# Optimization experiments

Measured on AMD Instinct MI355X. Metric: run time of the kernel, lower is better.

The kernel has to match this reference:

```python
import jax, jax.numpy as jnp
import numpy as np

B, L, D, H, A, NLAYERS, P = 16, 512, 768, 4, 100, 2, 3
DK = A // H  # 25
EPS = 1e-6


def setup_inputs() -> dict:
    key = jax.random.key(0)
    ks = jax.random.split(key, 20)
    s = 0.02
    return {
        "sequence_output": jax.random.normal(ks[0], (B, L, D), jnp.float32),
        "syntax_matrix": jax.random.normal(ks[1], (B, H, L, L), jnp.float32),
        # LayerNorm params
        "ln_a": jnp.ones((D,), jnp.float32),
        "ln_b": jnp.zeros((D,), jnp.float32),
        # Wxx: bert_dim -> attdim
        "Wxx_w": jax.random.normal(ks[2], (A, D), jnp.float32) * s,
        "Wxx_b": jnp.zeros((A,), jnp.float32),
        # attention q/k projections (attdim -> attdim)
        "q_w": jax.random.normal(ks[3], (A, A), jnp.float32) * s,
        "q_b": jnp.zeros((A,), jnp.float32),
        "k_w": jax.random.normal(ks[4], (A, A), jnp.float32) * s,
        "k_b": jnp.zeros((A,), jnp.float32),
        # W: attdim -> attdim
        "W_w": jax.random.normal(ks[5], (A, A), jnp.float32) * s,
        "W_b": jnp.zeros((A,), jnp.float32),
        # Wx: (H + 2*attdim) -> H
        "Wx_w": jax.random.normal(ks[6], (H, H + 2 * A), jnp.float32) * s,
        "Wx_b": jnp.zeros((H,), jnp.float32),
        # aggregate_W: attdim*(layers+1) -> attdim
        "agg_w": jax.random.normal(ks[7], (A, A * (NLAYERS + 1)), jnp.float32) * s,
        "agg_b": jnp.zeros((A,), jnp.float32),
        # classifier: 100 -> polarities_dim
        "cls_w": jax.random.normal(ks[8], (P, A), jnp.float32) * s,
        "cls_b": jnp.zeros((P,), jnp.float32),
        # masks (ints)
        "mask_ids": jnp.ones((B, L), jnp.int32),
        "src_mask": jnp.ones((B, L), jnp.int32),
    }


def reference(sequence_output, syntax_matrix, ln_a, ln_b, Wxx_w, Wxx_b,
              q_w, q_b, k_w, k_b, W_w, W_b, Wx_w, Wx_b,
              agg_w, agg_b, cls_w, cls_b, mask_ids, src_mask):
    # custom LayerNorm: torch.std is unbiased (ddof=1)
    mean = sequence_output.mean(-1, keepdims=True)
    std = jnp.std(sequence_output, axis=-1, ddof=1, keepdims=True)
    seq = ln_a * (sequence_output - mean) / (std + EPS) + ln_b

    # Wxx projection to attdim (dropout = identity in eval)
    x = seq @ Wxx_w.T + Wxx_b  # [B, L, A]

    # multi-head attention producing adjacency [B, H, L, L]
    q = (x @ q_w.T + q_b).reshape(B, L, H, DK).transpose(0, 2, 1, 3)
    k = (x @ k_w.T + k_b).reshape(B, L, H, DK).transpose(0, 2, 1, 3)
    scores = jnp.einsum('bhid,bhjd->bhij', q, k) / jnp.sqrt(jnp.float32(DK))
    key_mask = src_mask[:, None, None, :]  # [B,1,1,L]
    scores = jnp.where(key_mask == 0, jnp.float32(-1e9), scores)
    scores = scores + syntax_matrix
    adj = jax.nn.softmax(scores, axis=-1)  # [B, H, L, L]

    # split Wx into its adjacency / node-j / node-i blocks so the [B,L,L,H+2A]
    # concat tensor is never materialized (edge MLP is linear => decomposable)
    Aw = Wx_w[:, :H]            # [H, H]
    B1 = Wx_w[:, H:H + A]       # [H, A] applied to x[b, j]
    B2 = Wx_w[:, H + A:]        # [H, A] applied to x[b, i]

    x_g = x
    layer_list = [x]
    for i in range(NLAYERS):
        # Ax = mean over heads of adj_h @ x  (x identical per head)
        Ax = jnp.einsum('bhij,bjd->bid', adj, x_g) / H
        x_g = jax.nn.relu(Ax @ W_w.T + W_b)  # [B, L, A]
        layer_list.append(x_g)
        # edge update: edge[b,g,i,j] = sum_h Aw[g,h]*adj[b,h,i,j]
        e_adj = jnp.einsum('bhij,gh->bgij', adj, Aw)  # [B, H, L, L]
        u = jnp.einsum('bjd,gd->bgj', x_g, B1)        # node1 (index j)
        v = jnp.einsum('bid,gd->bgi', x_g, B2)        # node2 (index i)
        adj = e_adj + u[:, :, None, :] + v[:, :, :, None] + Wx_b[None, :, None, None]

    feats = jnp.concatenate(layer_list, axis=-1)          # [B, L, A*(NLAYERS+1)]
    node = jax.nn.relu(feats @ agg_w.T + agg_b)           # [B, L, A]

    valid_len = jnp.clip(mask_ids.sum(axis=1), 1, None).astype(node.dtype)[:, None]
    pooled = node.sum(axis=1) / valid_len                 # [B, A]
    logits = pooled @ cls_w.T + cls_b                     # [B, P]
    return logits
```

## Files before the change

kernel.cpp:

```cpp
#include <hip/hip_runtime.h>

#define B_ 16
#define L_ 512
#define D_ 768
#define H_ 4
#define A_ 100
#define DK_ 25
#define P_ 3
#define XP_ 128

__global__ __launch_bounds__(256) void k_wprep(const float* __restrict__ Wxx_w,
                                               float* __restrict__ wT)
{
    const int idx = blockIdx.x * 256 + threadIdx.x;
    const int d = idx >> 7, a = idx & 127;
    wT[idx] = (a < A_) ? Wxx_w[(size_t)a * D_ + d] : 0.f;
}

__global__ __launch_bounds__(256) void k_aggprep(const float* __restrict__ agg_w,
                                                 float* __restrict__ aggT)
{
    const int idx = blockIdx.x * 256 + threadIdx.x;
    const int n = idx & 127, k = (idx >> 7) % A_, c = idx / (128 * A_);
    aggT[idx] = (n < A_) ? agg_w[(size_t)n * (3 * A_) + c * A_ + k] : 0.f;
}

__global__ __launch_bounds__(256) void k_qkprep(const float* __restrict__ q_w,
                                                const float* __restrict__ k_w,
                                                float* __restrict__ qkT)
{
    const int idx = blockIdx.x * 256 + threadIdx.x;
    const int n = idx & 255, k = idx >> 8;
    const int half = n >> 7, a = n & 127;
    const float* w = half ? k_w : q_w;
    qkT[idx] = (a < A_) ? w[(size_t)a * A_ + k] : 0.f;
}

__global__ __launch_bounds__(256) void k_wprep2(const float* __restrict__ W_w,
                                                float* __restrict__ WT)
{
    const int idx = blockIdx.x * 256 + threadIdx.x;
    const int n = idx & 127, k = idx >> 7;
    WT[idx] = (n < A_) ? W_w[(size_t)n * A_ + k] : 0.f;
}

__global__ __launch_bounds__(256) void k_lnx(
    const float* __restrict__ seq, const float* __restrict__ ln_a, const float* __restrict__ ln_b,
    const float* __restrict__ wT, const float* __restrict__ Wxx_b, float* __restrict__ xp)
{
    __shared__ float ss[32][36];
    __shared__ float ws[32][128];
    __shared__ float mean_s[32], rd_s[32];
    const int tid = threadIdx.x;
    const int row0 = blockIdx.x * 32;
    const int wv = tid >> 6, lane = tid & 63;

    for (int rr = 0; rr < 8; ++rr) {
        const int r = wv * 8 + rr;
        const float4* src = (const float4*)(seq + (size_t)(row0 + r) * D_);
        float4 a = src[lane], b = src[lane + 64], c = src[lane + 128];
        float s = a.x + a.y + a.z + a.w + b.x + b.y + b.z + b.w + c.x + c.y + c.z + c.w;
        #pragma unroll
        for (int o = 32; o; o >>= 1) s += __shfl_xor(s, o);
        const float m = s * (1.0f / 768.0f);
        float q = (a.x-m)*(a.x-m) + (a.y-m)*(a.y-m) + (a.z-m)*(a.z-m) + (a.w-m)*(a.w-m)
                + (b.x-m)*(b.x-m) + (b.y-m)*(b.y-m) + (b.z-m)*(b.z-m) + (b.w-m)*(b.w-m)
                + (c.x-m)*(c.x-m) + (c.y-m)*(c.y-m) + (c.z-m)*(c.z-m) + (c.w-m)*(c.w-m);
        #pragma unroll
        for (int o = 32; o; o >>= 1) q += __shfl_xor(q, o);
        if (lane == 0) {
            mean_s[r] = m;
            rd_s[r] = 1.0f / (sqrtf(q * (1.0f / 767.0f)) + 1e-6f);
        }
    }
    __syncthreads();

    const int c4 = tid & 31, rg = tid >> 5;
    float4 acc[4];
    #pragma unroll
    for (int i = 0; i < 4; ++i) { acc[i].x = acc[i].y = acc[i].z = acc[i].w = 0.f; }

    for (int kc = 0; kc < 24; ++kc) {
        {
            const int r = tid >> 3, k4 = tid & 7;
            float4 v = *(const float4*)(seq + (size_t)(row0 + r) * D_ + kc * 32 + k4 * 4);
            float4 la = ((const float4*)ln_a)[kc * 8 + k4];
            float4 lb = ((const float4*)ln_b)[kc * 8 + k4];
            const float m = mean_s[r], rd = rd_s[r];
            float4 o;
            o.x = la.x * ((v.x - m) * rd) + lb.x;
            o.y = la.y * ((v.y - m) * rd) + lb.y;
            o.z = la.z * ((v.z - m) * rd) + lb.z;
            o.w = la.w * ((v.w - m) * rd) + lb.w;
            *(float4*)&ss[r][k4 * 4] = o;
        }
        #pragma unroll
        for (int t = 0; t < 4; ++t) {
            const int idx = tid + t * 256;
            const int k = idx >> 5, cc = idx & 31;
            *(float4*)&ws[k][cc * 4] = *(const float4*)(wT + (size_t)(kc * 32 + k) * 128 + cc * 4);
        }
        __syncthreads();
        #pragma unroll 2
        for (int k = 0; k < 32; k += 4) {
            float4 sv[4];
            #pragma unroll
            for (int i = 0; i < 4; ++i) sv[i] = *(float4*)&ss[rg * 4 + i][k];
            #pragma unroll
            for (int j = 0; j < 4; ++j) {
                float4 w4 = *(float4*)&ws[k + j][c4 * 4];
                #pragma unroll
                for (int i = 0; i < 4; ++i) {
                    const float sj = ((float*)&sv[i])[j];
                    acc[i].x += sj * w4.x; acc[i].y += sj * w4.y;
                    acc[i].z += sj * w4.z; acc[i].w += sj * w4.w;
                }
            }
        }
        __syncthreads();
    }

    float4 bias = {0.f, 0.f, 0.f, 0.f};
    if (c4 < 25) bias = ((const float4*)Wxx_b)[c4];
    #pragma unroll
    for (int i = 0; i < 4; ++i) {
        float4 o;
        o.x = acc[i].x + bias.x; o.y = acc[i].y + bias.y;
        o.z = acc[i].z + bias.z; o.w = acc[i].w + bias.w;
        *(float4*)(xp + (size_t)(row0 + rg * 4 + i) * XP_ + c4 * 4) = o;
    }
}

__global__ __launch_bounds__(256) void k_qkg(
    const float* __restrict__ xp, const float* __restrict__ qkT,
    const float* __restrict__ q_b, const float* __restrict__ k_b,
    float* __restrict__ qt, float* __restrict__ kt)
{
    __shared__ float ss[32][104];
    __shared__ float ws[A_][128];
    const int tid = threadIdx.x;
    const int row0 = blockIdx.x * 32;
    const int half = blockIdx.y;
    const int c4 = tid & 31, rg = tid >> 5;

    for (int idx = tid; idx < 32 * 25; idx += 256) {
        const int r = idx / 25, k4 = idx % 25;
        *(float4*)&ss[r][k4 * 4] = *(const float4*)(xp + (size_t)(row0 + r) * XP_ + k4 * 4);
    }
    for (int idx = tid; idx < A_ * 32; idx += 256) {
        const int k = idx >> 5, cc = idx & 31;
        *(float4*)&ws[k][cc * 4] = *(const float4*)(qkT + (size_t)k * 256 + half * 128 + cc * 4);
    }
    __syncthreads();

    float4 acc[4];
    #pragma unroll
    for (int i = 0; i < 4; ++i) { acc[i].x = acc[i].y = acc[i].z = acc[i].w = 0.f; }
    #pragma unroll 5
    for (int k = 0; k < A_; k += 4) {
        float4 sv[4];
        #pragma unroll
        for (int i = 0; i < 4; ++i) sv[i] = *(float4*)&ss[rg * 4 + i][k];
        #pragma unroll
        for (int j = 0; j < 4; ++j) {
            float4 w4 = *(float4*)&ws[k + j][c4 * 4];
            #pragma unroll
            for (int i = 0; i < 4; ++i) {
                const float sj = ((float*)&sv[i])[j];
                acc[i].x += sj * w4.x; acc[i].y += sj * w4.y;
                acc[i].z += sj * w4.z; acc[i].w += sj * w4.w;
            }
        }
    }

    if (c4 < 25) {
        const float4 bias = ((const float4*)(half ? k_b : q_b))[c4];
        float* dst = half ? kt : qt;
        #pragma unroll
        for (int i = 0; i < 4; ++i) {
            float4 o;
            o.x = acc[i].x + bias.x; o.y = acc[i].y + bias.y;
            o.z = acc[i].z + bias.z; o.w = acc[i].w + bias.w;
            *(float4*)(dst + (size_t)(row0 + rg * 4 + i) * A_ + c4 * 4) = o;
        }
    }
}

__global__ __launch_bounds__(256) void k_sgemm(
    const float* __restrict__ qt, const float* __restrict__ kt,
    const float* __restrict__ syn, const int* __restrict__ src_mask,
    float* __restrict__ es)
{
    __shared__ float qs[DK_][64];
    __shared__ float ks[DK_][64];
    __shared__ int ms[64];
    const int tid = threadIdx.x;
    const int bh = blockIdx.z;
    const int b = bh >> 2, h = bh & 3;
    const int i0 = blockIdx.x * 64, j0 = blockIdx.y * 64;
    const float* qbase = qt + ((size_t)b * L_ + i0) * A_ + h * DK_;
    const float* kbase = kt + ((size_t)b * L_ + j0) * A_ + h * DK_;
    {
        const int r = tid >> 2, c = tid & 3;
        #pragma unroll
        for (int k = 0; k < 7; ++k) {
            const int d = c + 4 * k;
            if (d < DK_) {
                qs[d][r] = qbase[(size_t)r * A_ + d];
                ks[d][r] = kbase[(size_t)r * A_ + d];
            }
        }
        if (tid < 64) ms[tid] = src_mask[b * L_ + j0 + tid];
    }
    __syncthreads();
    const int ty = tid >> 4, tx = tid & 15;
    float acc[4][4] = {};
    #pragma unroll 5
    for (int d = 0; d < DK_; ++d) {
        float4 qv = *(const float4*)&qs[d][ty * 4];
        float4 kv = *(const float4*)&ks[d][tx * 4];
        const float q[4] = {qv.x, qv.y, qv.z, qv.w};
        const float kk[4] = {kv.x, kv.y, kv.z, kv.w};
        #pragma unroll
        for (int ii = 0; ii < 4; ++ii)
            #pragma unroll
            for (int jj = 0; jj < 4; ++jj)
                acc[ii][jj] += q[ii] * kk[jj];
    }
    const int irow = i0 + ty * 4, jcol = j0 + tx * 4;
    const int m0 = ms[tx * 4], m1 = ms[tx * 4 + 1], m2 = ms[tx * 4 + 2], m3 = ms[tx * 4 + 3];
    #pragma unroll
    for (int ii = 0; ii < 4; ++ii) {
        const size_t o = ((size_t)bh * L_ + irow + ii) * L_ + jcol;
        float4 sv = *(const float4*)(syn + o);
        float4 w;
        w.x = (m0 ? acc[ii][0] * 0.2f : -1e9f) + sv.x;
        w.y = (m1 ? acc[ii][1] * 0.2f : -1e9f) + sv.y;
        w.z = (m2 ? acc[ii][2] * 0.2f : -1e9f) + sv.z;
        w.w = (m3 ? acc[ii][3] * 0.2f : -1e9f) + sv.w;
        *(float4*)(es + o) = w;
    }
}

__global__ __launch_bounds__(256) void k_softmax(
    const float* __restrict__ Wx_w, float* __restrict__ es)
{
    __shared__ float ps[H_][L_];
    __shared__ float cs[H_];
    const int tid = threadIdx.x, r = blockIdx.x;
    const int b = r >> 9, i = r & 511;
    const int h = tid >> 6, lane = tid & 63;
    if (tid < H_) cs[tid] = Wx_w[tid] + Wx_w[204 + tid] + Wx_w[408 + tid] + Wx_w[612 + tid];
    float* row = es + (((size_t)(b * H_ + h)) * L_ + i) * L_;
    float4 v0 = ((const float4*)row)[lane];
    float4 v1 = ((const float4*)row)[lane + 64];
    float mx = fmaxf(fmaxf(fmaxf(v0.x, v0.y), fmaxf(v0.z, v0.w)),
                     fmaxf(fmaxf(v1.x, v1.y), fmaxf(v1.z, v1.w)));
    #pragma unroll
    for (int o = 32; o; o >>= 1) mx = fmaxf(mx, __shfl_xor(mx, o));
    float4 e0, e1;
    e0.x = __expf(v0.x - mx); e0.y = __expf(v0.y - mx);
    e0.z = __expf(v0.z - mx); e0.w = __expf(v0.w - mx);
    e1.x = __expf(v1.x - mx); e1.y = __expf(v1.y - mx);
    e1.z = __expf(v1.z - mx); e1.w = __expf(v1.w - mx);
    float sum = e0.x + e0.y + e0.z + e0.w + e1.x + e1.y + e1.z + e1.w;
    #pragma unroll
    for (int o = 32; o; o >>= 1) sum += __shfl_xor(sum, o);
    const float inv = 1.0f / sum;
    e0.x *= inv; e0.y *= inv; e0.z *= inv; e0.w *= inv;
    e1.x *= inv; e1.y *= inv; e1.z *= inv; e1.w *= inv;
    *(float4*)&ps[h][lane * 4] = e0;
    *(float4*)&ps[h][(lane + 64) * 4] = e1;
    __syncthreads();
    float* arow = es + (((size_t)(b * H_ + 0)) * L_ + i) * L_;
    float* wrow = es + (((size_t)(b * H_ + 1)) * L_ + i) * L_;
    const int t = tid & 127;
    float4 p0 = *(float4*)&ps[0][t * 4];
    float4 p1 = *(float4*)&ps[1][t * 4];
    float4 p2 = *(float4*)&ps[2][t * 4];
    float4 p3 = *(float4*)&ps[3][t * 4];
    if (tid < 128) {
        float4 o;
        o.x = p0.x + p1.x + p2.x + p3.x;
        o.y = p0.y + p1.y + p2.y + p3.y;
        o.z = p0.z + p1.z + p2.z + p3.z;
        o.w = p0.w + p1.w + p2.w + p3.w;
        *(float4*)(arow + t * 4) = o;
    } else {
        const float c0 = cs[0], c1 = cs[1], c2 = cs[2], c3 = cs[3];
        float4 o;
        o.x = c0 * p0.x + c1 * p1.x + c2 * p2.x + c3 * p3.x;
        o.y = c0 * p0.y + c1 * p1.y + c2 * p2.y + c3 * p3.y;
        o.z = c0 * p0.z + c1 * p1.z + c2 * p2.z + c3 * p3.z;
        o.w = c0 * p0.w + c1 * p1.w + c2 * p2.w + c3 * p3.w;
        *(float4*)(wrow + t * 4) = o;
    }
}

template<int LAYER2>
__global__ __launch_bounds__(256) void k_axg(
    const float* __restrict__ adj, const float* __restrict__ xp,
    const float* __restrict__ S, const float* __restrict__ T,
    const float* __restrict__ Vv, const float* __restrict__ Wx_b,
    float* __restrict__ axb)
{
    __shared__ float ss[32][36];
    __shared__ float ws[32][128];
    const int tid = threadIdx.x;
    const int row0 = blockIdx.x * 32;
    const int b = row0 >> 9, i0 = row0 & 511;
    const float* adjb = adj + (size_t)b * 4 * L_ * L_;
    const int c4 = tid & 31, rg = tid >> 5;
    float4 acc[4];
    #pragma unroll
    for (int i = 0; i < 4; ++i) { acc[i].x = acc[i].y = acc[i].z = acc[i].w = 0.f; }

    for (int kc = 0; kc < 16; ++kc) {
        {
            const int r = tid >> 3, q4 = tid & 7;
            *(float4*)&ss[r][q4 * 4] =
                *(const float4*)(adjb + (size_t)(i0 + r) * L_ + kc * 32 + q4 * 4);
        }
        #pragma unroll
        for (int t = 0; t < 4; ++t) {
            const int idx = tid + t * 256;
            const int k = idx >> 5, cc = idx & 31;
            *(float4*)&ws[k][cc * 4] =
                *(const float4*)(xp + ((size_t)b * L_ + kc * 32 + k) * XP_ + cc * 4);
        }
        __syncthreads();
        #pragma unroll 2
        for (int k = 0; k < 32; k += 4) {
            float4 sv[4];
            #pragma unroll
            for (int i = 0; i < 4; ++i) sv[i] = *(float4*)&ss[rg * 4 + i][k];
            #pragma unroll
            for (int j = 0; j < 4; ++j) {
                float4 w4 = *(float4*)&ws[k + j][c4 * 4];
                #pragma unroll
                for (int i = 0; i < 4; ++i) {
                    const float sj = ((float*)&sv[i])[j];
                    acc[i].x += sj * w4.x; acc[i].y += sj * w4.y;
                    acc[i].z += sj * w4.z; acc[i].w += sj * w4.w;
                }
            }
        }
        __syncthreads();
    }

    float wb = 0.f;
    float4 Sv = {0.f, 0.f, 0.f, 0.f}, Tv = {0.f, 0.f, 0.f, 0.f};
    if (LAYER2) {
        wb = Wx_b[0] + Wx_b[1] + Wx_b[2] + Wx_b[3];
        if (c4 < 25) {
            Sv = ((const float4*)(S + b * A_))[c4];
            Tv = ((const float4*)(T + b * A_))[c4];
        }
    }
    #pragma unroll
    for (int i = 0; i < 4; ++i) {
        const int grow = row0 + rg * 4 + i;
        const float vv = LAYER2 ? (Vv[grow] + wb) : 0.f;
        float4 o;
        o.x = (acc[i].x + Sv.x + vv * Tv.x) * 0.25f;
        o.y = (acc[i].y + Sv.y + vv * Tv.y) * 0.25f;
        o.z = (acc[i].z + Sv.z + vv * Tv.z) * 0.25f;
        o.w = (acc[i].w + Sv.w + vv * Tv.w) * 0.25f;
        *(float4*)(axb + (size_t)grow * XP_ + c4 * 4) = o;
    }
}

__global__ __launch_bounds__(256) void k_xw(
    const float* __restrict__ axb, const float* __restrict__ WT,
    const float* __restrict__ W_b, float* __restrict__ xout)
{
    __shared__ float ss[32][104];
    __shared__ float ws[A_][128];
    const int tid = threadIdx.x;
    const int row0 = blockIdx.x * 32;
    const int c4 = tid & 31, rg = tid >> 5;

    for (int idx = tid; idx < 32 * 25; idx += 256) {
        const int r = idx / 25, k4 = idx % 25;
        *(float4*)&ss[r][k4 * 4] = *(const float4*)(axb + (size_t)(row0 + r) * XP_ + k4 * 4);
    }
    for (int idx = tid; idx < A_ * 32; idx += 256) {
        const int k = idx >> 5, cc = idx & 31;
        *(float4*)&ws[k][cc * 4] = *(const float4*)(WT + (size_t)k * 128 + cc * 4);
    }
    __syncthreads();

    float4 acc[4];
    #pragma unroll
    for (int i = 0; i < 4; ++i) { acc[i].x = acc[i].y = acc[i].z = acc[i].w = 0.f; }
    #pragma unroll 5
    for (int k = 0; k < A_; k += 4) {
        float4 sv[4];
        #pragma unroll
        for (int i = 0; i < 4; ++i) sv[i] = *(float4*)&ss[rg * 4 + i][k];
        #pragma unroll
        for (int j = 0; j < 4; ++j) {
            float4 w4 = *(float4*)&ws[k + j][c4 * 4];
            #pragma unroll
            for (int i = 0; i < 4; ++i) {
                const float sj = ((float*)&sv[i])[j];
                acc[i].x += sj * w4.x; acc[i].y += sj * w4.y;
                acc[i].z += sj * w4.z; acc[i].w += sj * w4.w;
            }
        }
    }

    float4 bias = {0.f, 0.f, 0.f, 0.f};
    if (c4 < 25) bias = ((const float4*)W_b)[c4];
    #pragma unroll
    for (int i = 0; i < 4; ++i) {
        float4 o;
        o.x = fmaxf(acc[i].x + bias.x, 0.f); o.y = fmaxf(acc[i].y + bias.y, 0.f);
        o.z = fmaxf(acc[i].z + bias.z, 0.f); o.w = fmaxf(acc[i].w + bias.w, 0.f);
        *(float4*)(xout + (size_t)(row0 + rg * 4 + i) * XP_ + c4 * 4) = o;
    }
}

__global__ __launch_bounds__(256) void k_extras(
    const float* __restrict__ x1, const float* __restrict__ Wx_w,
    float* __restrict__ Vv, float* __restrict__ T, float* __restrict__ S,
    float* __restrict__ pooled)
{
    __shared__ float b1s[A_], b2s[A_], Ul[L_];
    const int tid = threadIdx.x, b = blockIdx.x;
    if (tid < A_) {
        float s1 = 0.f, s2 = 0.f;
        #pragma unroll
        for (int g = 0; g < H_; ++g) {
            s1 += Wx_w[g * 204 + 4 + tid];
            s2 += Wx_w[g * 204 + 104 + tid];
        }
        b1s[tid] = s1; b2s[tid] = s2;
        pooled[b * A_ + tid] = 0.f;
    }
    __syncthreads();
    for (int j = tid; j < L_; j += 256) {
        const float* xr = x1 + ((size_t)b * L_ + j) * XP_;
        float u = 0.f, v = 0.f;
        #pragma unroll 4
        for (int c = 0; c < A_; ++c) { float xv = xr[c]; u += xv * b1s[c]; v += xv * b2s[c]; }
        Ul[j] = u;
        Vv[b * L_ + j] = v;
    }
    __syncthreads();
    if (tid < A_) {
        float t = 0.f, s = 0.f;
        for (int j = 0; j < L_; ++j) {
            float xv = x1[((size_t)b * L_ + j) * XP_ + tid];
            t += xv; s += Ul[j] * xv;
        }
        T[b * A_ + tid] = t; S[b * A_ + tid] = s;
    }
}

__global__ __launch_bounds__(256) void k_nodepool(
    const float* __restrict__ x, const float* __restrict__ x1, const float* __restrict__ x2,
    const float* __restrict__ aggT, const float* __restrict__ agg_b,
    float* __restrict__ pooled)
{
    __shared__ float ss[32][104];
    __shared__ float ws[A_][128];
    const int tid = threadIdx.x;
    const int row0 = blockIdx.x * 32;
    const int b = row0 >> 9;
    const int c4 = tid & 31, rg = tid >> 5;
    float4 acc[4];
    #pragma unroll
    for (int i = 0; i < 4; ++i) { acc[i].x = acc[i].y = acc[i].z = acc[i].w = 0.f; }

    for (int c = 0; c < 3; ++c) {
        const float* src = (c == 0) ? x : (c == 1) ? x1 : x2;
        for (int idx = tid; idx < 32 * 25; idx += 256) {
            const int r = idx / 25, k4 = idx % 25;
            *(float4*)&ss[r][k4 * 4] =
                *(const float4*)(src + (size_t)(row0 + r) * XP_ + k4 * 4);
        }
        for (int idx = tid; idx < A_ * 32; idx += 256) {
            const int k = idx >> 5, cc = idx & 31;
            *(float4*)&ws[k][cc * 4] =
                *(const float4*)(aggT + ((size_t)c * A_ + k) * 128 + cc * 4);
        }
        __syncthreads();
        #pragma unroll 5
        for (int k = 0; k < A_; k += 4) {
            float4 sv[4];
            #pragma unroll
            for (int i = 0; i < 4; ++i) sv[i] = *(float4*)&ss[rg * 4 + i][k];
            #pragma unroll
            for (int j = 0; j < 4; ++j) {
                float4 w4 = *(float4*)&ws[k + j][c4 * 4];
                #pragma unroll
                for (int i = 0; i < 4; ++i) {
                    const float sj = ((float*)&sv[i])[j];
                    acc[i].x += sj * w4.x; acc[i].y += sj * w4.y;
                    acc[i].z += sj * w4.z; acc[i].w += sj * w4.w;
                }
            }
        }
        __syncthreads();
    }

    float4 bias = {0.f, 0.f, 0.f, 0.f};
    if (c4 < 25) bias = ((const float4*)agg_b)[c4];
    float4 rs = {0.f, 0.f, 0.f, 0.f};
    #pragma unroll
    for (int i = 0; i < 4; ++i) {
        rs.x += fmaxf(acc[i].x + bias.x, 0.f);
        rs.y += fmaxf(acc[i].y + bias.y, 0.f);
        rs.z += fmaxf(acc[i].z + bias.z, 0.f);
        rs.w += fmaxf(acc[i].w + bias.w, 0.f);
    }
    float* red = &ss[0][0];
    __syncthreads();
    *(float4*)&red[rg * 128 + c4 * 4] = rs;
    __syncthreads();
    if (rg == 0 && c4 < 25) {
        float4 tot = {0.f, 0.f, 0.f, 0.f};
        #pragma unroll
        for (int g = 0; g < 8; ++g) {
            float4 v = *(float4*)&red[g * 128 + c4 * 4];
            tot.x += v.x; tot.y += v.y; tot.z += v.z; tot.w += v.w;
        }
        atomicAdd(&pooled[b * A_ + c4 * 4 + 0], tot.x);
        atomicAdd(&pooled[b * A_ + c4 * 4 + 1], tot.y);
        atomicAdd(&pooled[b * A_ + c4 * 4 + 2], tot.z);
        atomicAdd(&pooled[b * A_ + c4 * 4 + 3], tot.w);
    }
}

__global__ __launch_bounds__(64) void k_logits(
    const float* __restrict__ pooled, const float* __restrict__ cls_w,
    const float* __restrict__ cls_b, const int* __restrict__ mask_ids,
    float* __restrict__ out)
{
    const int tid = threadIdx.x;
    if (tid < B_ * P_) {
        const int b = tid / P_, p = tid % P_;
        int vs = 0;
        for (int l = 0; l < L_; ++l) vs += mask_ids[b * L_ + l];
        float inv = 1.0f / (float)max(vs, 1);
        float acc = cls_b[p];
        #pragma unroll 4
        for (int a = 0; a < A_; ++a) acc += (pooled[b * A_ + a] * inv) * cls_w[p * A_ + a];
        out[b * P_ + p] = acc;
    }
}

extern "C" void kernel_launch(void* const* d_in, const int* in_sizes, int n_in,
                              void* d_out, int out_size, void* d_ws, size_t ws_size,
                              hipStream_t stream) {
    const float* seq    = (const float*)d_in[0];
    const float* syn    = (const float*)d_in[1];
    const float* ln_a   = (const float*)d_in[2];
    const float* ln_b   = (const float*)d_in[3];
    const float* Wxx_w  = (const float*)d_in[4];
    const float* Wxx_b  = (const float*)d_in[5];
    const float* q_w    = (const float*)d_in[6];
    const float* q_b    = (const float*)d_in[7];
    const float* k_w    = (const float*)d_in[8];
    const float* k_b    = (const float*)d_in[9];
    const float* W_w    = (const float*)d_in[10];
    const float* W_b    = (const float*)d_in[11];
    const float* Wx_w   = (const float*)d_in[12];
    const float* Wx_b   = (const float*)d_in[13];
    const float* agg_w  = (const float*)d_in[14];
    const float* agg_b  = (const float*)d_in[15];
    const float* cls_w  = (const float*)d_in[16];
    const float* cls_b  = (const float*)d_in[17];
    const int* mask_ids = (const int*)d_in[18];
    const int* src_mask = (const int*)d_in[19];
    float* out = (float*)d_out;

    float* ws = (float*)d_ws;
    size_t off = 0;
    float* xp     = ws + off; off += (size_t)B_ * L_ * XP_;
    float* x1p    = ws + off; off += (size_t)B_ * L_ * XP_;
    float* x2p    = ws + off; off += (size_t)B_ * L_ * XP_;
    float* axb    = ws + off; off += (size_t)B_ * L_ * XP_;
    float* qt     = ws + off; off += (size_t)B_ * L_ * A_;
    float* kt     = ws + off; off += (size_t)B_ * L_ * A_;
    float* es     = ws + off; off += (size_t)B_ * H_ * L_ * L_;
    float* Vv     = ws + off; off += (size_t)B_ * L_;
    float* T      = ws + off; off += (size_t)B_ * A_;
    float* S      = ws + off; off += (size_t)B_ * A_;
    float* pooled = ws + off; off += (size_t)B_ * A_;
    float* wT     = ws + off; off += (size_t)D_ * 128;
    float* aggT   = ws + off; off += (size_t)3 * A_ * 128;
    float* qkT    = ws + off; off += (size_t)A_ * 256;
    float* WT     = ws + off; off += (size_t)A_ * 128;

    k_wprep<<<(D_ * 128) / 256, 256, 0, stream>>>(Wxx_w, wT);
    k_aggprep<<<(3 * A_ * 128) / 256, 256, 0, stream>>>(agg_w, aggT);
    k_qkprep<<<(A_ * 256) / 256, 256, 0, stream>>>(q_w, k_w, qkT);
    k_wprep2<<<(A_ * 128) / 256, 256, 0, stream>>>(W_w, WT);
    k_lnx<<<(B_ * L_) / 32, 256, 0, stream>>>(seq, ln_a, ln_b, wT, Wxx_b, xp);
    k_qkg<<<dim3((B_ * L_) / 32, 2), 256, 0, stream>>>(xp, qkT, q_b, k_b, qt, kt);
    k_sgemm<<<dim3(8, 8, B_ * H_), 256, 0, stream>>>(qt, kt, syn, src_mask, es);
    k_softmax<<<B_ * L_, 256, 0, stream>>>(Wx_w, es);
    k_axg<0><<<(B_ * L_) / 32, 256, 0, stream>>>(es, xp, nullptr, nullptr, nullptr, nullptr, axb);
    k_xw<<<(B_ * L_) / 32, 256, 0, stream>>>(axb, WT, W_b, x1p);
    k_extras<<<B_, 256, 0, stream>>>(x1p, Wx_w, Vv, T, S, pooled);
    k_axg<1><<<(B_ * L_) / 32, 256, 0, stream>>>(es + (size_t)L_ * L_, x1p, S, T, Vv, Wx_b, axb);
    k_xw<<<(B_ * L_) / 32, 256, 0, stream>>>(axb, WT, W_b, x2p);
    k_nodepool<<<(B_ * L_) / 32, 256, 0, stream>>>(xp, x1p, x2p, aggT, agg_b, pooled);
    k_logits<<<1, 64, 0, stream>>>(pooled, cls_w, cls_b, mask_ids, out);
}
```

Before: 401.8 us.

## Double-buffer LDS tiles via async global-to-LDS loads and fold LayerNorm into epilogue

Replaces the register-staged tile loads in k_lnx and k_axg with async global_load_lds DMA into double-buffered LDS, prefetching the next K-chunk while the current one is computed. LayerNorm is folded algebraically: ln_a is pre-multiplied into the weight, and mean/rstd corrections use a precomputed column sum and bias vector in the epilogue, so raw inputs can be DMA'd directly. This removes the per-tile normalize pass and one barrier per iteration. It also drops the LDS padding, which may add bank conflicts, and the single-thread-per-column k_vecprep kernel adds a small serial prep launch.

After: 413.2 us. 2.8% more time.

```diff
diff --git a/kernel.cpp b/kernel.cpp
--- a/kernel.cpp
+++ b/kernel.cpp
@@ -9,12 +9,42 @@
 #define P_ 3
 #define XP_ 128
 
+typedef unsigned int u32_t;
+typedef const u32_t __attribute__((address_space(1)))* gas_t;
+typedef u32_t __attribute__((address_space(3)))* las_t;
+__device__ __forceinline__ void dma16(const float* g, float* l) {
+    __builtin_amdgcn_global_load_lds((gas_t)g, (las_t)l, 16, 0, 0);
+}
+
 __global__ __launch_bounds__(256) void k_wprep(const float* __restrict__ Wxx_w,
+                                               const float* __restrict__ ln_a,
                                                float* __restrict__ wT)
 {
     const int idx = blockIdx.x * 256 + threadIdx.x;
     const int d = idx >> 7, a = idx & 127;
-    wT[idx] = (a < A_) ? Wxx_w[(size_t)a * D_ + d] : 0.f;
+    wT[idx] = (a < A_) ? ln_a[d] * Wxx_w[(size_t)a * D_ + d] : 0.f;
+}
+
+__global__ __launch_bounds__(128) void k_vecprep(const float* __restrict__ Wxx_w,
+                                                 const float* __restrict__ ln_a,
+                                                 const float* __restrict__ ln_b,
+                                                 const float* __restrict__ Wxx_b,
+                                                 float* __restrict__ colsum,
+                                                 float* __restrict__ basev)
+{
+    const int a = threadIdx.x;
+    float cs = 0.f, bs = 0.f;
+    if (a < A_) {
+        const float* wr = Wxx_w + (size_t)a * D_;
+        for (int d = 0; d < D_; ++d) {
+            const float w = wr[d];
+            cs += ln_a[d] * w;
+            bs += ln_b[d] * w;
+        }
+        bs += Wxx_b[a];
+    }
+    colsum[a] = (a < A_) ? cs : 0.f;
+    basev[a]  = (a < A_) ? bs : 0.f;
 }
 
 __global__ __launch_bounds__(256) void k_aggprep(const float* __restrict__ agg_w,
@@ -45,11 +75,12 @@
 }
 
 __global__ __launch_bounds__(256) void k_lnx(
-    const float* __restrict__ seq, const float* __restrict__ ln_a, const float* __restrict__ ln_b,
-    const float* __restrict__ wT, const float* __restrict__ Wxx_b, float* __restrict__ xp)
-{
-    __shared__ float ss[32][36];
-    __shared__ float ws[32][128];
+    const float* __restrict__ seq, const float* __restrict__ wT,
+    const float* __restrict__ colsum, const float* __restrict__ basev,
+    float* __restrict__ xp)
+{
+    __shared__ float ss[2][32][32];
+    __shared__ float ws[2][32][128];
     __shared__ float mean_s[32], rd_s[32];
     const int tid = threadIdx.x;
     const int row0 = blockIdx.x * 32;
@@ -73,42 +104,40 @@
             rd_s[r] = 1.0f / (sqrtf(q * (1.0f / 767.0f)) + 1e-6f);
         }
     }
-    __syncthreads();
 
     const int c4 = tid & 31, rg = tid >> 5;
     float4 acc[4];
     #pragma unroll
     for (int i = 0; i < 4; ++i) { acc[i].x = acc[i].y = acc[i].z = acc[i].w = 0.f; }
 
+    const int sr = tid >> 3, sk = (tid & 7) * 4;
+    dma16(seq + (size_t)(row0 + sr) * D_ + sk, &ss[0][0][0] + tid * 4);
+    #pragma unroll
+    for (int t = 0; t < 4; ++t) {
+        const int idx = tid + t * 256;
+        dma16(wT + idx * 4, &ws[0][0][0] + idx * 4);
+    }
+    __syncthreads();
+
     for (int kc = 0; kc < 24; ++kc) {
-        {
-            const int r = tid >> 3, k4 = tid & 7;
-            float4 v = *(const float4*)(seq + (size_t)(row0 + r) * D_ + kc * 32 + k4 * 4);
-            float4 la = ((const float4*)ln_a)[kc * 8 + k4];
-            float4 lb = ((const float4*)ln_b)[kc * 8 + k4];
-            const float m = mean_s[r], rd = rd_s[r];
-            float4 o;
-            o.x = la.x * ((v.x - m) * rd) + lb.x;
-            o.y = la.y * ((v.y - m) * rd) + lb.y;
-            o.z = la.z * ((v.z - m) * rd) + lb.z;
-            o.w = la.w * ((v.w - m) * rd) + lb.w;
-            *(float4*)&ss[r][k4 * 4] = o;
-        }
-        #pragma unroll
-        for (int t = 0; t < 4; ++t) {
-            const int idx = tid + t * 256;
-            const int k = idx >> 5, cc = idx & 31;
-            *(float4*)&ws[k][cc * 4] = *(const float4*)(wT + (size_t)(kc * 32 + k) * 128 + cc * 4);
-        }
-        __syncthreads();
-        #pragma unroll 2
+        const int cur = kc & 1;
+        if (kc < 23) {
+            dma16(seq + (size_t)(row0 + sr) * D_ + (kc + 1) * 32 + sk,
+                  &ss[cur ^ 1][0][0] + tid * 4);
+            #pragma unroll
+            for (int t = 0; t < 4; ++t) {
+                const int idx = tid + t * 256;
+                dma16(wT + (size_t)(kc + 1) * 4096 + idx * 4, &ws[cur ^ 1][0][0] + idx * 4);
+            }
+        }
+        #pragma unroll
         for (int k = 0; k < 32; k += 4) {
             float4 sv[4];
             #pragma unroll
-            for (int i = 0; i < 4; ++i) sv[i] = *(float4*)&ss[rg * 4 + i][k];
+            for (int i = 0; i < 4; ++i) sv[i] = *(float4*)&ss[cur][rg * 4 + i][k];
             #pragma unroll
             for (int j = 0; j < 4; ++j) {
-                float4 w4 = *(float4*)&ws[k + j][c4 * 4];
+                float4 w4 = *(float4*)&ws[cur][k + j][c4 * 4];
                 #pragma unroll
                 for (int i = 0; i < 4; ++i) {
                     const float sj = ((float*)&sv[i])[j];
@@ -120,14 +149,18 @@
         __syncthreads();
     }
 
-    float4 bias = {0.f, 0.f, 0.f, 0.f};
-    if (c4 < 25) bias = ((const float4*)Wxx_b)[c4];
+    const float4 cs4 = ((const float4*)colsum)[c4];
+    const float4 bs4 = ((const float4*)basev)[c4];
     #pragma unroll
     for (int i = 0; i < 4; ++i) {
+        const int r = rg * 4 + i;
+        const float m = mean_s[r], rd = rd_s[r];
         float4 o;
-        o.x = acc[i].x + bias.x; o.y = acc[i].y + bias.y;
-        o.z = acc[i].z + bias.z; o.w = acc[i].w + bias.w;
-        *(float4*)(xp + (size_t)(row0 + rg * 4 + i) * XP_ + c4 * 4) = o;
+        o.x = rd * (acc[i].x - m * cs4.x) + bs4.x;
+        o.y = rd * (acc[i].y - m * cs4.y) + bs4.y;
+        o.z = rd * (acc[i].z - m * cs4.z) + bs4.z;
+        o.w = rd * (acc[i].w - m * cs4.w) + bs4.w;
+        *(float4*)(xp + (size_t)(row0 + r) * XP_ + c4 * 4) = o;
     }
 }
 
@@ -304,39 +337,46 @@
     const float* __restrict__ Vv, const float* __restrict__ Wx_b,
     float* __restrict__ axb)
 {
-    __shared__ float ss[32][36];
-    __shared__ float ws[32][128];
+    __shared__ float ss[2][32][32];
+    __shared__ float ws[2][32][128];
     const int tid = threadIdx.x;
     const int row0 = blockIdx.x * 32;
     const int b = row0 >> 9, i0 = row0 & 511;
     const float* adjb = adj + (size_t)b * 4 * L_ * L_;
+    const float* xpb = xp + (size_t)b * L_ * XP_;
     const int c4 = tid & 31, rg = tid >> 5;
     float4 acc[4];
     #pragma unroll
     for (int i = 0; i < 4; ++i) { acc[i].x = acc[i].y = acc[i].z = acc[i].w = 0.f; }
 
+    const int sr = tid >> 3, sk = (tid & 7) * 4;
+    dma16(adjb + (size_t)(i0 + sr) * L_ + sk, &ss[0][0][0] + tid * 4);
+    #pragma unroll
+    for (int t = 0; t < 4; ++t) {
+        const int idx = tid + t * 256;
+        dma16(xpb + idx * 4, &ws[0][0][0] + idx * 4);
+    }
+    __syncthreads();
+
     for (int kc = 0; kc < 16; ++kc) {
-        {
-            const int r = tid >> 3, q4 = tid & 7;
-            *(float4*)&ss[r][q4 * 4] =
-                *(const float4*)(adjb + (size_t)(i0 + r) * L_ + kc * 32 + q4 * 4);
-        }
-        #pragma unroll
-        for (int t = 0; t < 4; ++t) {
-            const int idx = tid + t * 256;
-            const int k = idx >> 5, cc = idx & 31;
-            *(float4*)&ws[k][cc * 4] =
-                *(const float4*)(xp + ((size_t)b * L_ + kc * 32 + k) * XP_ + cc * 4);
-        }
-        __syncthreads();
-        #pragma unroll 2
+        const int cur = kc & 1;
+        if (kc < 15) {
+            dma16(adjb + (size_t)(i0 + sr) * L_ + (kc + 1) * 32 + sk,
+                  &ss[cur ^ 1][0][0] + tid * 4);
+            #pragma unroll
+            for (int t = 0; t < 4; ++t) {
+                const int idx = tid + t * 256;
+                dma16(xpb + (size_t)(kc + 1) * 4096 + idx * 4, &ws[cur ^ 1][0][0] + idx * 4);
+            }
+        }
+        #pragma unroll
         for (int k = 0; k < 32; k += 4) {
             float4 sv[4];
             #pragma unroll
-            for (int i = 0; i < 4; ++i) sv[i] = *(float4*)&ss[rg * 4 + i][k];
+            for (int i = 0; i < 4; ++i) sv[i] = *(float4*)&ss[cur][rg * 4 + i][k];
             #pragma unroll
             for (int j = 0; j < 4; ++j) {
-                float4 w4 = *(float4*)&ws[k + j][c4 * 4];
+                float4 w4 = *(float4*)&ws[cur][k + j][c4 * 4];
                 #pragma unroll
                 for (int i = 0; i < 4; ++i) {
                     const float sj = ((float*)&sv[i])[j];
@@ -593,12 +633,15 @@
     float* aggT   = ws + off; off += (size_t)3 * A_ * 128;
     float* qkT    = ws + off; off += (size_t)A_ * 256;
     float* WT     = ws + off; off += (size_t)A_ * 128;
-
-    k_wprep<<<(D_ * 128) / 256, 256, 0, stream>>>(Wxx_w, wT);
+    float* colsum = ws + off; off += 128;
+    float* basev  = ws + off; off += 128;
+
+    k_wprep<<<(D_ * 128) / 256, 256, 0, stream>>>(Wxx_w, ln_a, wT);
+    k_vecprep<<<1, 128, 0, stream>>>(Wxx_w, ln_a, ln_b, Wxx_b, colsum, basev);
     k_aggprep<<<(3 * A_ * 128) / 256, 256, 0, stream>>>(agg_w, aggT);
     k_qkprep<<<(A_ * 256) / 256, 256, 0, stream>>>(q_w, k_w, qkT);
     k_wprep2<<<(A_ * 128) / 256, 256, 0, stream>>>(W_w, WT);
-    k_lnx<<<(B_ * L_) / 32, 256, 0, stream>>>(seq, ln_a, ln_b, wT, Wxx_b, xp);
+    k_lnx<<<(B_ * L_) / 32, 256, 0, stream>>>(seq, wT, colsum, basev, xp);
     k_qkg<<<dim3((B_ * L_) / 32, 2), 256, 0, stream>>>(xp, qkT, q_b, k_b, qt, kt);
     k_sgemm<<<dim3(8, 8, B_ * H_), 256, 0, stream>>>(qt, kt, syn, src_mask, es);
     k_softmax<<<B_ * L_, 256, 0, stream>>>(Wx_w, es);
```
